# Optimization experiments

Measured on AMD Instinct MI355X. Metric: run time of the kernel, lower is better.

## Reference

```python
import jax, jax.numpy as jnp
import numpy as np

NUM_HEADS = 32
NUM_KV_HEADS = 8
HEAD_DIM = 128


def setup_inputs() -> dict:
    key = jax.random.key(0)
    ks = jax.random.split(key, 5)
    B, S, H = 1, 2048, 4096
    hidden_states = jax.random.normal(ks[0], (B, S, H), dtype=jnp.float32)
    # additive causal mask: 0 on/below diagonal, large negative above
    neg = jnp.finfo(jnp.float32).min
    causal = jnp.where(jnp.tril(jnp.ones((S, S), dtype=bool)), 0.0, neg)
    attention_mask = causal[None, None, :, :].astype(jnp.float32)
    sc = 0.02
    wq = jax.random.normal(ks[1], (NUM_HEADS * HEAD_DIM, H), dtype=jnp.float32) * sc
    wk = jax.random.normal(ks[2], (NUM_KV_HEADS * HEAD_DIM, H), dtype=jnp.float32) * sc
    wv = jax.random.normal(ks[3], (NUM_KV_HEADS * HEAD_DIM, H), dtype=jnp.float32) * sc
    wo = jax.random.normal(ks[4], (H, NUM_HEADS * HEAD_DIM), dtype=jnp.float32) * sc
    return {"hidden_states": hidden_states, "attention_mask": attention_mask,
            "wq": wq, "wk": wk, "wv": wv, "wo": wo}


def reference(hidden_states, attention_mask, wq, wk, wv, wo):
    B, S, H = hidden_states.shape
    groups = NUM_HEADS // NUM_KV_HEADS
    # projections (Linear, no bias): y = x @ W^T
    q = (hidden_states @ wq.T).reshape(B, S, NUM_HEADS, HEAD_DIM).transpose(0, 2, 1, 3)
    k = (hidden_states @ wk.T).reshape(B, S, NUM_KV_HEADS, HEAD_DIM).transpose(0, 2, 1, 3)
    v = (hidden_states @ wv.T).reshape(B, S, NUM_KV_HEADS, HEAD_DIM).transpose(0, 2, 1, 3)
    # GQA: repeat KV heads (matches torch repeat_interleave on head dim)
    k = jnp.repeat(k, groups, axis=1)  # [B, NUM_HEADS, S, D]
    v = jnp.repeat(v, groups, axis=1)
    scale = 1.0 / (HEAD_DIM ** 0.5)
    scores = jnp.einsum('bhqd,bhkd->bhqk', q, k) * scale
    scores = scores + attention_mask
    attn = jax.nn.softmax(scores.astype(jnp.float32), axis=-1).astype(q.dtype)
    out = jnp.einsum('bhqk,bhkd->bhqd', attn, v)  # [B, H, S, D]
    out = out.transpose(0, 2, 1, 3).reshape(B, S, NUM_HEADS * HEAD_DIM)
    return out @ wo.T
```

## Files before the change

kernel.cpp:

```cpp
#include <hip/hip_runtime.h>
#include <hip/hip_bf16.h>
#include <cstdint>
#include <cstddef>

typedef __bf16 bf16;
typedef __bf16 bf16x4 __attribute__((ext_vector_type(4)));
typedef __bf16 bf16x8 __attribute__((ext_vector_type(8)));
typedef float  f32x4  __attribute__((ext_vector_type(4)));

#define S_LEN 2048
#define HID   4096
#define NH    32
#define NKV   8
#define HD    128
#define QLD   6144
#define KVLD  6144

__device__ __forceinline__ void gload_lds16(const bf16* g, bf16* l) {
    __builtin_amdgcn_global_load_lds(
        (const __attribute__((address_space(1))) void*)g,
        (__attribute__((address_space(3))) void*)l,
        16, 0, 0);
}

__global__ void cast_f32_bf16(const float* __restrict__ in, bf16* __restrict__ out, int n4) {
    int idx    = blockIdx.x * blockDim.x + threadIdx.x;
    int stride = gridDim.x * blockDim.x;
    for (int i = idx; i < n4; i += stride) {
        float4 v = ((const float4*)in)[i];
        bf16x4 o = { (bf16)v.x, (bf16)v.y, (bf16)v.z, (bf16)v.w };
        ((bf16x4*)out)[i] = o;
    }
}

template <typename OUT_T>
__global__ __launch_bounds__(256) void gemm_bt(const bf16* __restrict__ A,
                                               const bf16* __restrict__ B,
                                               OUT_T* __restrict__ C,
                                               int M, int N, int K) {
    __shared__ alignas(16) bf16 sA[2][128 * 64];
    __shared__ alignas(16) bf16 sB[2][128 * 64];

    const int tid  = threadIdx.x;
    const int lane = tid & 63;
    const int w    = tid >> 6;
    const int wr   = w >> 1;
    const int wc   = w & 1;
    const int l15  = lane & 15;
    const int l4   = lane >> 4;
    const int mt   = M >> 7;
    const int m0   = (blockIdx.x % mt) * 128;
    const int n0   = (blockIdx.x / mt) * 128;

    f32x4 acc[4][4] = {};

    const int rsub = lane >> 3;
    const int scol = ((lane & 7) * 8) ^ (rsub << 3);

    auto stage = [&](int t, int buf) {
#pragma unroll
        for (int j = 0; j < 4; ++j) {
            const int c   = w * 4 + j;
            const int row = c * 8 + rsub;
            gload_lds16(A + (size_t)(m0 + row) * K + t * 64 + scol, &sA[buf][c * 512]);
            gload_lds16(B + (size_t)(n0 + row) * K + t * 64 + scol, &sB[buf][c * 512]);
        }
    };

    const int nt = K >> 6;

    stage(0, 0);
    __syncthreads();

    int buf = 0;
    for (int t = 0; t < nt; ++t) {
        if (t + 1 < nt) stage(t + 1, buf ^ 1);

        bf16x8 af[2][4], bfr[2][4];
#pragma unroll
        for (int kk = 0; kk < 2; ++kk) {
#pragma unroll
            for (int i = 0; i < 4; ++i) {
                const int ra = wr * 64 + i * 16 + l15;
                af[kk][i]  = *(const bf16x8*)&sA[buf][ra * 64 + ((kk * 32 + l4 * 8) ^ ((ra & 7) << 3))];
                const int rb = wc * 64 + i * 16 + l15;
                bfr[kk][i] = *(const bf16x8*)&sB[buf][rb * 64 + ((kk * 32 + l4 * 8) ^ ((rb & 7) << 3))];
            }
        }
#pragma unroll
        for (int kk = 0; kk < 2; ++kk)
#pragma unroll
            for (int i = 0; i < 4; ++i)
#pragma unroll
                for (int j = 0; j < 4; ++j)
                    acc[i][j] = __builtin_amdgcn_mfma_f32_16x16x32_bf16(af[kk][i], bfr[kk][j], acc[i][j], 0, 0, 0);

        __syncthreads();
        buf ^= 1;
    }

#pragma unroll
    for (int i = 0; i < 4; ++i) {
        const int row = m0 + wr * 64 + i * 16 + l4 * 4;
#pragma unroll
        for (int j = 0; j < 4; ++j) {
            const int col = n0 + wc * 64 + j * 16 + l15;
#pragma unroll
            for (int r = 0; r < 4; ++r)
                C[(size_t)(row + r) * N + col] = (OUT_T)acc[i][j][r];
        }
    }
}

__global__ __launch_bounds__(512) void attn_kernel(const bf16* __restrict__ Q,
                                                   const bf16* __restrict__ Kp,
                                                   const bf16* __restrict__ Vp,
                                                   bf16* __restrict__ O) {
    __shared__ alignas(16) bf16 sK[2][64 * 128];
    __shared__ alignas(16) bf16 sVt[2][128 * 64];
    __shared__ alignas(16) bf16 sP[8][16 * 64];

    const int tid  = threadIdx.x;
    const int lane = tid & 63;
    const int w    = tid >> 6;
    const int l15  = lane & 15;
    const int l4   = lane >> 4;
    const int h    = blockIdx.y;
    const int hk   = h >> 2;
    const int b    = blockIdx.x;
    const int qH   = 15 - b;
    const int qL   = b;
    const float C2 = 0.12751744f;

    const bf16* Kbase = Kp + hk * HD;
    const bf16* Vbase = Vp + hk * HD;

    const int rbH = qH * 128 + w * 16;
    const int rbL = qL * 128 + w * 16;
    bf16x8 qfH[4], qfL[4];
#pragma unroll
    for (int ks = 0; ks < 4; ++ks) {
        qfH[ks] = *(const bf16x8*)(Q + (size_t)(rbH + l15) * QLD + h * HD + ks * 32 + l4 * 8);
        qfL[ks] = *(const bf16x8*)(Q + (size_t)(rbL + l15) * QLD + h * HD + ks * 32 + l4 * 8);
    }

    f32x4 accH[8] = {}, accL[8] = {};
    float lH[4] = {0.f, 0.f, 0.f, 0.f}, lL[4] = {0.f, 0.f, 0.f, 0.f};

    auto stageK = [&](int t, int buf) {
#pragma unroll
        for (int j = 0; j < 2; ++j) {
            const int c   = w * 2 + j;
            const int row = c * 4 + l4;
            const int col = (l15 * 8) ^ ((row & 7) << 3);
            gload_lds16(Kbase + (size_t)(t * 64 + row) * KVLD + col, &sK[buf][c * 512]);
        }
    };
    auto loadV = [&](int t, bf16x8* vr) {
#pragma unroll
        for (int r2 = 0; r2 < 2; ++r2) {
            const int c = r2 * 8 + w;
            vr[r2] = *(const bf16x8*)(Vbase + (size_t)(t * 64 + lane) * KVLD + c * 8);
        }
    };
    auto writeV = [&](const bf16x8* vr, int buf) {
#pragma unroll
        for (int r2 = 0; r2 < 2; ++r2) {
            const int c = r2 * 8 + w;
#pragma unroll
            for (int e = 0; e < 8; ++e) {
                const int row = c * 8 + e;
                sVt[buf][row * 64 + (lane ^ (e << 3))] = vr[r2][e];
            }
        }
    };

    auto strip = [&](const bf16x8* qf, f32x4* acc_o, float* lrow,
                     int rbase, int s0, int cur) {
        if (s0 > rbase + 15) return;
        f32x4 accs[4] = {};
        __builtin_amdgcn_s_setprio(1);
#pragma unroll
        for (int ks = 0; ks < 4; ++ks) {
#pragma unroll
            for (int j = 0; j < 4; ++j) {
                const int krow = j * 16 + l15;
                bf16x8 kb = *(const bf16x8*)&sK[cur][krow * 128 + ((ks * 32 + l4 * 8) ^ ((krow & 7) << 3))];
                accs[j] = __builtin_amdgcn_mfma_f32_16x16x32_bf16(qf[ks], kb, accs[j], 0, 0, 0);
            }
        }
        __builtin_amdgcn_s_setprio(0);

        float sc[4][4];
        float rsum[4] = {0.f, 0.f, 0.f, 0.f};
        const bool needMask = (s0 + 63 > rbase);
        if (needMask) {
#pragma unroll
            for (int j = 0; j < 4; ++j) {
                const int scol = s0 + j * 16 + l15;
#pragma unroll
                for (int i = 0; i < 4; ++i) {
                    const int r = rbase + l4 * 4 + i;
                    const float p = (scol > r) ? 0.f : exp2f(accs[j][i] * C2);
                    sc[j][i] = p;
                    rsum[i] += p;
                }
            }
        } else {
#pragma unroll
            for (int j = 0; j < 4; ++j)
#pragma unroll
                for (int i = 0; i < 4; ++i) {
                    const float p = exp2f(accs[j][i] * C2);
                    sc[j][i] = p;
                    rsum[i] += p;
                }
        }
#pragma unroll
        for (int i = 0; i < 4; ++i) {
#pragma unroll
            for (int msk = 1; msk < 16; msk <<= 1)
                rsum[i] += __shfl_xor(rsum[i], msk);
            lrow[i] += rsum[i];
        }

#pragma unroll
        for (int j = 0; j < 4; ++j)
#pragma unroll
            for (int i = 0; i < 4; ++i) {
                const int prow = l4 * 4 + i;
                const int s2   = (prow & 7) ^ ((prow >> 3) << 1);
                sP[w][prow * 64 + ((j * 16 + l15) ^ (s2 << 3))] = (bf16)sc[j][i];
            }

        __builtin_amdgcn_s_setprio(1);
#pragma unroll
        for (int kk = 0; kk < 2; ++kk) {
            const int s2l = (l15 & 7) ^ ((l15 >> 3) << 1);
            bf16x8 pa = *(const bf16x8*)&sP[w][l15 * 64 + ((kk * 32 + l4 * 8) ^ (s2l << 3))];
#pragma unroll
            for (int d = 0; d < 8; ++d) {
                const int vrow = d * 16 + l15;
                bf16x8 vb = *(const bf16x8*)&sVt[cur][vrow * 64 + ((kk * 32 + l4 * 8) ^ ((vrow & 7) << 3))];
                acc_o[d] = __builtin_amdgcn_mfma_f32_16x16x32_bf16(pa, vb, acc_o[d], 0, 0, 0);
            }
        }
        __builtin_amdgcn_s_setprio(0);
    };

    const int ntH = 2 * qH + 2;
    const int ntL = 2 * qL + 2;

    bf16x8 vreg[2];
    loadV(0, vreg);
    stageK(0, 0);
    writeV(vreg, 0);
    __syncthreads();

    int cur = 0;
    for (int t = 0; t < ntH; ++t) {
        const int s0 = t * 64;
        const bool pf = (t + 1 < ntH);
        if (pf) {
            loadV(t + 1, vreg);
            stageK(t + 1, cur ^ 1);
        }

        strip(qfH, accH, lH, rbH, s0, cur);
        if (t < ntL) strip(qfL, accL, lL, rbL, s0, cur);

        if (pf) writeV(vreg, cur ^ 1);

        __syncthreads();
        cur ^= 1;
    }

    float rH[4], rL[4];
#pragma unroll
    for (int i = 0; i < 4; ++i) { rH[i] = __frcp_rn(lH[i]); rL[i] = __frcp_rn(lL[i]); }
#pragma unroll
    for (int d = 0; d < 8; ++d)
#pragma unroll
        for (int i = 0; i < 4; ++i) {
            O[(size_t)(rbH + l4 * 4 + i) * HID + h * HD + d * 16 + l15] = (bf16)(accH[d][i] * rH[i]);
            O[(size_t)(rbL + l4 * 4 + i) * HID + h * HD + d * 16 + l15] = (bf16)(accL[d][i] * rL[i]);
        }
}

extern "C" void kernel_launch(void* const* d_in, const int* in_sizes, int n_in,
                              void* d_out, int out_size, void* d_ws, size_t ws_size,
                              hipStream_t stream) {
    const float* hx = (const float*)d_in[0];
    const float* wq = (const float*)d_in[2];
    const float* wk = (const float*)d_in[3];
    const float* wv = (const float*)d_in[4];
    const float* wo = (const float*)d_in[5];
    float* out = (float*)d_out;

    bf16* Xb   = (bf16*)d_ws;
    bf16* Wqkv = Xb + 8388608;
    bf16* QKV  = Wqkv + 25165824;

    auto cast = [&](const float* src, bf16* dst, int n) {
        int n4 = n / 4;
        int blocks = (n4 + 255) / 256;
        if (blocks > 2048) blocks = 2048;
        cast_f32_bf16<<<blocks, 256, 0, stream>>>(src, dst, n4);
    };

    cast(hx, Xb, 2048 * 4096);
    cast(wq, Wqkv, 4096 * 4096);
    cast(wk, Wqkv + 16777216, 1024 * 4096);
    cast(wv, Wqkv + 20971520, 1024 * 4096);

    gemm_bt<bf16><<<dim3(768), 256, 0, stream>>>(Xb, Wqkv, QKV, 2048, 6144, 4096);

    cast(wo, Wqkv, 4096 * 4096);

    attn_kernel<<<dim3(8, 32), 512, 0, stream>>>(QKV, QKV + 4096, QKV + 5120, Xb);

    gemm_bt<float><<<dim3(512), 256, 0, stream>>>(Xb, Wqkv, out, 2048, 4096, 4096);
}
```

Before: 322.8 us.

## Split attention into 64-row strips per warp-half and remap GEMM blocks across XCDs

The attention kernel now launches 16 blocks per head instead of 8. Each block pairs a high and a low 64-row query strip, with warps 0-3 taking one strip and warps 4-7 the other. Previously every warp processed two 16-row strips, so this halves per-warp register state and doubles the number of blocks, while keeping the causal work per block balanced. The GEMM block index is also permuted so that consecutive tiles land on the same XCD (chiplet), aiming for better L2 reuse. The risk is that K/V tiles are now staged once per 64-row pair rather than once per 128-row pair, which doubles K/V load traffic per head.

```diff
diff --git a/kernel.cpp b/kernel.cpp
--- a/kernel.cpp
+++ b/kernel.cpp
@@ -49,8 +49,10 @@
     const int l15  = lane & 15;
     const int l4   = lane >> 4;
     const int mt   = M >> 7;
-    const int m0   = (blockIdx.x % mt) * 128;
-    const int n0   = (blockIdx.x / mt) * 128;
+    const int cpx  = (int)gridDim.x >> 3;
+    const int vb   = (blockIdx.x & 7) * cpx + (blockIdx.x >> 3);
+    const int m0   = (vb % mt) * 128;
+    const int n0   = (vb / mt) * 128;
 
     f32x4 acc[4][4] = {};
 
@@ -128,24 +130,22 @@
     const int h    = blockIdx.y;
     const int hk   = h >> 2;
     const int b    = blockIdx.x;
-    const int qH   = 15 - b;
-    const int qL   = b;
+    const int qs   = (w < 4) ? (31 - b) : b;
+    const int wl   = w & 3;
+    const int rbase = qs * 64 + wl * 16;
+    const int myNt  = qs + 1;
     const float C2 = 0.12751744f;
 
     const bf16* Kbase = Kp + hk * HD;
     const bf16* Vbase = Vp + hk * HD;
 
-    const int rbH = qH * 128 + w * 16;
-    const int rbL = qL * 128 + w * 16;
-    bf16x8 qfH[4], qfL[4];
-#pragma unroll
-    for (int ks = 0; ks < 4; ++ks) {
-        qfH[ks] = *(const bf16x8*)(Q + (size_t)(rbH + l15) * QLD + h * HD + ks * 32 + l4 * 8);
-        qfL[ks] = *(const bf16x8*)(Q + (size_t)(rbL + l15) * QLD + h * HD + ks * 32 + l4 * 8);
-    }
-
-    f32x4 accH[8] = {}, accL[8] = {};
-    float lH[4] = {0.f, 0.f, 0.f, 0.f}, lL[4] = {0.f, 0.f, 0.f, 0.f};
+    bf16x8 qf[4];
+#pragma unroll
+    for (int ks = 0; ks < 4; ++ks)
+        qf[ks] = *(const bf16x8*)(Q + (size_t)(rbase + l15) * QLD + h * HD + ks * 32 + l4 * 8);
+
+    f32x4 acc_o[8] = {};
+    float lrow[4] = {0.f, 0.f, 0.f, 0.f};
 
     auto stageK = [&](int t, int buf) {
 #pragma unroll
@@ -175,81 +175,7 @@
         }
     };
 
-    auto strip = [&](const bf16x8* qf, f32x4* acc_o, float* lrow,
-                     int rbase, int s0, int cur) {
-        if (s0 > rbase + 15) return;
-        f32x4 accs[4] = {};
-        __builtin_amdgcn_s_setprio(1);
-#pragma unroll
-        for (int ks = 0; ks < 4; ++ks) {
-#pragma unroll
-            for (int j = 0; j < 4; ++j) {
-                const int krow = j * 16 + l15;
-                bf16x8 kb = *(const bf16x8*)&sK[cur][krow * 128 + ((ks * 32 + l4 * 8) ^ ((krow & 7) << 3))];
-                accs[j] = __builtin_amdgcn_mfma_f32_16x16x32_bf16(qf[ks], kb, accs[j], 0, 0, 0);
-            }
-        }
-        __builtin_amdgcn_s_setprio(0);
-
-        float sc[4][4];
-        float rsum[4] = {0.f, 0.f, 0.f, 0.f};
-        const bool needMask = (s0 + 63 > rbase);
-        if (needMask) {
-#pragma unroll
-            for (int j = 0; j < 4; ++j) {
-                const int scol = s0 + j * 16 + l15;
-#pragma unroll
-                for (int i = 0; i < 4; ++i) {
-                    const int r = rbase + l4 * 4 + i;
-                    const float p = (scol > r) ? 0.f : exp2f(accs[j][i] * C2);
-                    sc[j][i] = p;
-                    rsum[i] += p;
-                }
-            }
-        } else {
-#pragma unroll
-            for (int j = 0; j < 4; ++j)
-#pragma unroll
-                for (int i = 0; i < 4; ++i) {
-                    const float p = exp2f(accs[j][i] * C2);
-                    sc[j][i] = p;
-                    rsum[i] += p;
-                }
-        }
-#pragma unroll
-        for (int i = 0; i < 4; ++i) {
-#pragma unroll
-            for (int msk = 1; msk < 16; msk <<= 1)
-                rsum[i] += __shfl_xor(rsum[i], msk);
-            lrow[i] += rsum[i];
-        }
-
-#pragma unroll
-        for (int j = 0; j < 4; ++j)
-#pragma unroll
-            for (int i = 0; i < 4; ++i) {
-                const int prow = l4 * 4 + i;
-                const int s2   = (prow & 7) ^ ((prow >> 3) << 1);
-                sP[w][prow * 64 + ((j * 16 + l15) ^ (s2 << 3))] = (bf16)sc[j][i];
-            }
-
-        __builtin_amdgcn_s_setprio(1);
-#pragma unroll
-        for (int kk = 0; kk < 2; ++kk) {
-            const int s2l = (l15 & 7) ^ ((l15 >> 3) << 1);
-            bf16x8 pa = *(const bf16x8*)&sP[w][l15 * 64 + ((kk * 32 + l4 * 8) ^ (s2l << 3))];
-#pragma unroll
-            for (int d = 0; d < 8; ++d) {
-                const int vrow = d * 16 + l15;
-                bf16x8 vb = *(const bf16x8*)&sVt[cur][vrow * 64 + ((kk * 32 + l4 * 8) ^ ((vrow & 7) << 3))];
-                acc_o[d] = __builtin_amdgcn_mfma_f32_16x16x32_bf16(pa, vb, acc_o[d], 0, 0, 0);
-            }
-        }
-        __builtin_amdgcn_s_setprio(0);
-    };
-
-    const int ntH = 2 * qH + 2;
-    const int ntL = 2 * qL + 2;
+    const int ntH = 32 - b;
 
     bf16x8 vreg[2];
     loadV(0, vreg);
@@ -266,8 +192,76 @@
             stageK(t + 1, cur ^ 1);
         }
 
-        strip(qfH, accH, lH, rbH, s0, cur);
-        if (t < ntL) strip(qfL, accL, lL, rbL, s0, cur);
+        if (t < myNt) {
+            f32x4 accs[4] = {};
+            __builtin_amdgcn_s_setprio(1);
+#pragma unroll
+            for (int ks = 0; ks < 4; ++ks) {
+#pragma unroll
+                for (int j = 0; j < 4; ++j) {
+                    const int krow = j * 16 + l15;
+                    bf16x8 kb = *(const bf16x8*)&sK[cur][krow * 128 + ((ks * 32 + l4 * 8) ^ ((krow & 7) << 3))];
+                    accs[j] = __builtin_amdgcn_mfma_f32_16x16x32_bf16(qf[ks], kb, accs[j], 0, 0, 0);
+                }
+            }
+            __builtin_amdgcn_s_setprio(0);
+
+            float sc[4][4];
+            float rsum[4] = {0.f, 0.f, 0.f, 0.f};
+            const bool needMask = (s0 + 63 > rbase);
+            if (needMask) {
+#pragma unroll
+                for (int j = 0; j < 4; ++j) {
+                    const int scol = s0 + j * 16 + l15;
+#pragma unroll
+                    for (int i = 0; i < 4; ++i) {
+                        const int r = rbase + l4 * 4 + i;
+                        const float p = (scol > r) ? 0.f : exp2f(accs[j][i] * C2);
+                        sc[j][i] = p;
+                        rsum[i] += p;
+                    }
+                }
+            } else {
+#pragma unroll
+                for (int j = 0; j < 4; ++j)
+#pragma unroll
+                    for (int i = 0; i < 4; ++i) {
+                        const float p = exp2f(accs[j][i] * C2);
+                        sc[j][i] = p;
+                        rsum[i] += p;
+                    }
+            }
+#pragma unroll
+            for (int i = 0; i < 4; ++i) {
+#pragma unroll
+                for (int msk = 1; msk < 16; msk <<= 1)
+                    rsum[i] += __shfl_xor(rsum[i], msk);
+                lrow[i] += rsum[i];
+            }
+
+#pragma unroll
+            for (int j = 0; j < 4; ++j)
+#pragma unroll
+                for (int i = 0; i < 4; ++i) {
+                    const int prow = l4 * 4 + i;
+                    const int s2   = (prow & 7) ^ ((prow >> 3) << 1);
+                    sP[w][prow * 64 + ((j * 16 + l15) ^ (s2 << 3))] = (bf16)sc[j][i];
+                }
+
+            __builtin_amdgcn_s_setprio(1);
+#pragma unroll
+            for (int kk = 0; kk < 2; ++kk) {
+                const int s2l = (l15 & 7) ^ ((l15 >> 3) << 1);
+                bf16x8 pa = *(const bf16x8*)&sP[w][l15 * 64 + ((kk * 32 + l4 * 8) ^ (s2l << 3))];
+#pragma unroll
+                for (int d = 0; d < 8; ++d) {
+                    const int vrow = d * 16 + l15;
+                    bf16x8 vb = *(const bf16x8*)&sVt[cur][vrow * 64 + ((kk * 32 + l4 * 8) ^ ((vrow & 7) << 3))];
+                    acc_o[d] = __builtin_amdgcn_mfma_f32_16x16x32_bf16(pa, vb, acc_o[d], 0, 0, 0);
+                }
+            }
+            __builtin_amdgcn_s_setprio(0);
+        }
 
         if (pf) writeV(vreg, cur ^ 1);
 
@@ -275,16 +269,14 @@
         cur ^= 1;
     }
 
-    float rH[4], rL[4];
-#pragma unroll
-    for (int i = 0; i < 4; ++i) { rH[i] = __frcp_rn(lH[i]); rL[i] = __frcp_rn(lL[i]); }
+    float rinv[4];
+#pragma unroll
+    for (int i = 0; i < 4; ++i) rinv[i] = __frcp_rn(lrow[i]);
 #pragma unroll
     for (int d = 0; d < 8; ++d)
 #pragma unroll
-        for (int i = 0; i < 4; ++i) {
-            O[(size_t)(rbH + l4 * 4 + i) * HID + h * HD + d * 16 + l15] = (bf16)(accH[d][i] * rH[i]);
-            O[(size_t)(rbL + l4 * 4 + i) * HID + h * HD + d * 16 + l15] = (bf16)(accL[d][i] * rL[i]);
-        }
+        for (int i = 0; i < 4; ++i)
+            O[(size_t)(rbase + l4 * 4 + i) * HID + h * HD + d * 16 + l15] = (bf16)(acc_o[d][i] * rinv[i]);
 }
 
 extern "C" void kernel_launch(void* const* d_in, const int* in_sizes, int n_in,
@@ -317,7 +309,7 @@
 
     cast(wo, Wqkv, 4096 * 4096);
 
-    attn_kernel<<<dim3(8, 32), 512, 0, stream>>>(QKV, QKV + 4096, QKV + 5120, Xb);
+    attn_kernel<<<dim3(16, 32), 512, 0, stream>>>(QKV, QKV + 4096, QKV + 5120, Xb);
 
     gemm_bt<float><<<dim3(512), 256, 0, stream>>>(Xb, Wqkv, out, 2048, 4096, 4096);
 }
```

Measured after the change: 366.5 us. 1.14x slower.
